# Kernel optimization log

Hardware: AMD Instinct MI355X
Metric: run time of the kernel (lower is better)

The kernel has to match this reference:

```python
import jax, jax.numpy as jnp
import numpy as np

SEGMENT_LENGTHS = [2048, 4096, 8192]
DILATION_RATES = [1, 2, 4]


def setup_inputs() -> dict:
    key = jax.random.key(0)
    kq, kk, kv = jax.random.split(key, 3)
    shape = (4, 8192, 16, 64)  # [b, seq, heads, head_dim]
    return {
        "query": jax.random.normal(kq, shape, dtype=jnp.float32),
        "key": jax.random.normal(kk, shape, dtype=jnp.float32),
        "value": jax.random.normal(kv, shape, dtype=jnp.float32),
    }


def _dilated_attention(query, key, value):
    b, S, h, d = query.shape
    num_groups = len(DILATION_RATES)
    # replicate torch group-size logic: h // ng each, first (h % ng) get +1
    group_sizes = [h // num_groups] * num_groups
    for i in range(h % num_groups):
        group_sizes[i] += 1

    scale = 1.0 / jnp.sqrt(jnp.asarray(d, dtype=query.dtype))
    out = jnp.zeros_like(query)

    for i, (g, r, s) in enumerate(zip(group_sizes, DILATION_RATES, SEGMENT_LENGTHS)):
        n = S // s
        offset = i % r
        hmin, hmax = i * g, (i + 1) * g  # faithful to original (uses current g)

        # gather strided segment views: [b, n, s', g, d]
        q = query.reshape(b, n, s, h, d)[:, :, offset::r, hmin:hmax, :]
        k = key.reshape(b, n, s, h, d)[:, :, offset::r, hmin:hmax, :]
        v = value.reshape(b, n, s, h, d)[:, :, offset::r, hmin:hmax, :]

        # NOTE: the original SDPA is applied to [., s', g, d], so attention
        # runs over the HEAD-group axis (length g) at each position.
        scores = jnp.einsum('bnsqd,bnskd->bnsqk', q, k) * scale
        attn = jax.nn.softmax(scores, axis=-1)
        x = jnp.einsum('bnsqk,bnskd->bnsqd', attn, v)  # [b, n, s', g, d]

        # normalize over (segment, position) dims, as in original
        x = x / x.sum(axis=(1, 2), keepdims=True)

        # scatter-add back into the output buffer
        out5 = out.reshape(b, n, s, h, d)
        out5 = out5.at[:, :, offset::r, hmin:hmax, :].add(x)
        out = out5.reshape(b, S, h, d)

    return out / num_groups


def reference(query, key, value):
    return _dilated_attention(query, key, value)
```

## Files before the change

### kernel.cpp

```cpp
#include <hip/hip_runtime.h>
#include <math.h>

#define BB 4
#define SS 8192
#define HH 16
#define DDIM 64

static const long X0_OFF = 6144;
static const long X0_SZ = 4L * 8192 * 6 * 64;
static const long X1_OFF = X0_OFF + X0_SZ;
static const long X1_SZ = 4L * 4096 * 5 * 64;
static const long X2_OFF = X1_OFF + X1_SZ;
static const long X2_SZ = 4L * 2048 * 5 * 64;
static const long WS_FLOATS = X2_OFF + X2_SZ;

__global__ __launch_bounds__(256) void k_zero_sums(float* ws) {
    int idx = blockIdx.x * 256 + threadIdx.x;
    if (idx < 6144) ws[idx] = 0.0f;
}

__global__ __launch_bounds__(256) void k_recip(float* ws) {
    int idx = blockIdx.x * 256 + threadIdx.x;
    if (idx < 6144) ws[idx] = __frcp_rn(ws[idx]);
}

__device__ __forceinline__ float4 shfl_xor4(float4 v, int m) {
    return make_float4(__shfl_xor(v.x, m, 64), __shfl_xor(v.y, m, 64),
                       __shfl_xor(v.z, m, 64), __shfl_xor(v.w, m, 64));
}

__global__ __launch_bounds__(256) void k_attn(const float* __restrict__ Q,
                                              const float* __restrict__ Kp,
                                              const float* __restrict__ Vp,
                                              float* __restrict__ ws) {
    __shared__ __align__(16) float psum[4][6][64];

    int bid = blockIdx.x;
    int gi, b, tile, g, r, off, hmin, J;
    long xoff;
    if (bid < 2048)      { gi = 0; b = bid >> 9; tile = bid & 511; g = 6; r = 1; off = 0; hmin = 0;  J = 8192; xoff = X0_OFF; }
    else if (bid < 3072) { gi = 1; bid -= 2048; b = bid >> 8; tile = bid & 255; g = 5; r = 2; off = 1; hmin = 5;  J = 4096; xoff = X1_OFF; }
    else                 { gi = 2; bid -= 3072; b = bid >> 7; tile = bid & 127; g = 5; r = 4; off = 2; hmin = 10; J = 2048; xoff = X2_OFF; }

    const int t = threadIdx.x;
    const int lane = t & 63;
    const int wave = t >> 6;
    const int d4 = t & 15;
    const int pIdx = t >> 4;
    const int j = tile * 16 + pIdx;
    const int pos = off + j * r;

    const long rowbase = (((long)b * SS + pos) * HH + hmin) * DDIM;
    const float4* q4p = (const float4*)(Q + rowbase);
    const float4* k4p = (const float4*)(Kp + rowbase);
    const float4* v4p = (const float4*)(Vp + rowbase);

    float4 q4[6], k4[6], v4[6];
#pragma unroll
    for (int hh = 0; hh < 6; ++hh) {
        if (hh < g) {
            q4[hh] = q4p[hh * 16 + d4];
            k4[hh] = k4p[hh * 16 + d4];
            v4[hh] = v4p[hh * 16 + d4];
        } else {
            q4[hh] = make_float4(0.f, 0.f, 0.f, 0.f);
            k4[hh] = q4[hh];
            v4[hh] = q4[hh];
        }
    }

    float p[6][6];
#pragma unroll
    for (int qh = 0; qh < 6; ++qh) {
#pragma unroll
        for (int kh = 0; kh < 6; ++kh) {
            if (qh < g && kh < g) {
                float s = q4[qh].x * k4[kh].x + q4[qh].y * k4[kh].y +
                          q4[qh].z * k4[kh].z + q4[qh].w * k4[kh].w;
#pragma unroll
                for (int m = 1; m <= 8; m <<= 1) s += __shfl_xor(s, m, 64);
                p[qh][kh] = s;
            } else {
                p[qh][kh] = 0.0f;
            }
        }
    }

#pragma unroll
    for (int qh = 0; qh < 6; ++qh) {
        if (qh >= g) continue;
        float mx = -3.4e38f;
#pragma unroll
        for (int kh = 0; kh < 6; ++kh)
            if (kh < g) mx = fmaxf(mx, p[qh][kh]);
        float den = 0.0f;
#pragma unroll
        for (int kh = 0; kh < 6; ++kh) {
            if (kh < g) { p[qh][kh] = __expf((p[qh][kh] - mx) * 0.125f); den += p[qh][kh]; }
        }
        float rden = 1.0f / den;
#pragma unroll
        for (int kh = 0; kh < 6; ++kh) p[qh][kh] *= rden;
    }

    float4* xrow = (float4*)(ws + xoff + (((long)b * J + j) * g) * DDIM);
#pragma unroll
    for (int qh = 0; qh < 6; ++qh) {
        if (qh >= g) continue;
        float4 o = make_float4(0.f, 0.f, 0.f, 0.f);
#pragma unroll
        for (int kh = 0; kh < 6; ++kh) {
            if (kh < g) {
                o.x += p[qh][kh] * v4[kh].x; o.y += p[qh][kh] * v4[kh].y;
                o.z += p[qh][kh] * v4[kh].z; o.w += p[qh][kh] * v4[kh].w;
            }
        }
        xrow[qh * 16 + d4] = o;

        float4 red = o;
        red = shfl_xor4(red, 16);
        {
            float4 tmp = shfl_xor4(red, 32);
            red.x += tmp.x; red.y += tmp.y; red.z += tmp.z; red.w += tmp.w;
        }
        red = o;
#pragma unroll
        for (int m = 16; m <= 32; m <<= 1) {
            float4 tmp = shfl_xor4(red, m);
            red.x += tmp.x; red.y += tmp.y; red.z += tmp.z; red.w += tmp.w;
        }
        if (lane < 16) ((float4*)&psum[wave][qh][0])[d4] = red;
    }
    __syncthreads();

    for (int idx = t; idx < g * 64; idx += 256) {
        int qh = idx >> 6, dd = idx & 63;
        float v = psum[0][qh][dd] + psum[1][qh][dd] + psum[2][qh][dd] + psum[3][qh][dd];
        unsafeAtomicAdd(ws + ((long)(gi * 4 + b) * 8 + qh) * 64 + dd, v);
    }
}

__global__ __launch_bounds__(256) void k_out(const float* __restrict__ ws,
                                             float* __restrict__ out) {
    const int t = threadIdx.x;
    const int bid = blockIdx.x;
    const int dd4 = t & 15;
    const int h = t >> 4;
    const int b = bid >> 10;
    const int pos0 = (bid & 1023) * 8;

    float4 rs0 = make_float4(0.f, 0.f, 0.f, 0.f), rs1 = rs0, rs2 = rs0;
    if (h < 6)
        rs0 = ((const float4*)(ws + ((long)(0 * 4 + b) * 8 + h) * 64))[dd4];
    if (h >= 5 && h <= 9)
        rs1 = ((const float4*)(ws + ((long)(1 * 4 + b) * 8 + (h - 5)) * 64))[dd4];
    if (h >= 10 && h <= 14)
        rs2 = ((const float4*)(ws + ((long)(2 * 4 + b) * 8 + (h - 10)) * 64))[dd4];

#pragma unroll
    for (int pp = 0; pp < 8; ++pp) {
        const int pos = pos0 + pp;
        float4 r = make_float4(0.f, 0.f, 0.f, 0.f);

        if (h < 6) {
            float4 x = ((const float4*)(ws + X0_OFF + (((long)b * 8192 + pos) * 6 + h) * 64))[dd4];
            r.x += x.x * rs0.x; r.y += x.y * rs0.y; r.z += x.z * rs0.z; r.w += x.w * rs0.w;
        }
        if (h >= 5 && h <= 9 && (pos & 1) == 1) {
            int jj = pos >> 1;
            float4 x = ((const float4*)(ws + X1_OFF + (((long)b * 4096 + jj) * 5 + (h - 5)) * 64))[dd4];
            r.x += x.x * rs1.x; r.y += x.y * rs1.y; r.z += x.z * rs1.z; r.w += x.w * rs1.w;
        }
        if (h >= 10 && h <= 14 && (pos & 3) == 2) {
            int jj = pos >> 2;
            float4 x = ((const float4*)(ws + X2_OFF + (((long)b * 2048 + jj) * 5 + (h - 10)) * 64))[dd4];
            r.x += x.x * rs2.x; r.y += x.y * rs2.y; r.z += x.z * rs2.z; r.w += x.w * rs2.w;
        }

        const float third = 1.0f / 3.0f;
        r.x *= third; r.y *= third; r.z *= third; r.w *= third;
        ((float4*)out)[((long)(b * 8192 + pos)) * 256 + t] = r;
    }
}

extern "C" void kernel_launch(void* const* d_in, const int* in_sizes, int n_in,
                              void* d_out, int out_size, void* d_ws, size_t ws_size,
                              hipStream_t stream) {
    const float* Q = (const float*)d_in[0];
    const float* K = (const float*)d_in[1];
    const float* V = (const float*)d_in[2];
    float* ws = (float*)d_ws;
    float* out = (float*)d_out;

    if (ws_size < (size_t)WS_FLOATS * sizeof(float)) return;

    k_zero_sums<<<24, 256, 0, stream>>>(ws);
    k_attn<<<3584, 256, 0, stream>>>(Q, K, V, ws);
    k_recip<<<24, 256, 0, stream>>>(ws);
    k_out<<<4096, 256, 0, stream>>>(ws, out);
}
```

Before: 403.0 us.

## Recompute attention in output kernel instead of materializing intermediates

The first pass now only accumulates the per-(group,batch,head,dim) normalization sums and no longer writes the full attention outputs to workspace. A new fused kernel recomputes the head-group attention per position, applies the reciprocal of the sums (folding the separate reciprocal kernel into it) and writes the final output directly. This trades a large intermediate write plus reread (~40MB each way) for rereading Q/K/V and redoing the small attention arithmetic, and removes one kernel launch.

New measurement: 441.6 us. +9.6%, slower.

```diff
diff --git a/kernel.cpp b/kernel.cpp
--- a/kernel.cpp
+++ b/kernel.cpp
@@ -6,41 +6,29 @@
 #define HH 16
 #define DDIM 64
 
-static const long X0_OFF = 6144;
-static const long X0_SZ = 4L * 8192 * 6 * 64;
-static const long X1_OFF = X0_OFF + X0_SZ;
-static const long X1_SZ = 4L * 4096 * 5 * 64;
-static const long X2_OFF = X1_OFF + X1_SZ;
-static const long X2_SZ = 4L * 2048 * 5 * 64;
-static const long WS_FLOATS = X2_OFF + X2_SZ;
+static const long WS_FLOATS = 6144;
 
 __global__ __launch_bounds__(256) void k_zero_sums(float* ws) {
     int idx = blockIdx.x * 256 + threadIdx.x;
     if (idx < 6144) ws[idx] = 0.0f;
 }
 
-__global__ __launch_bounds__(256) void k_recip(float* ws) {
-    int idx = blockIdx.x * 256 + threadIdx.x;
-    if (idx < 6144) ws[idx] = __frcp_rn(ws[idx]);
-}
-
 __device__ __forceinline__ float4 shfl_xor4(float4 v, int m) {
     return make_float4(__shfl_xor(v.x, m, 64), __shfl_xor(v.y, m, 64),
                        __shfl_xor(v.z, m, 64), __shfl_xor(v.w, m, 64));
 }
 
-__global__ __launch_bounds__(256) void k_attn(const float* __restrict__ Q,
-                                              const float* __restrict__ Kp,
-                                              const float* __restrict__ Vp,
-                                              float* __restrict__ ws) {
+__global__ __launch_bounds__(256) void k_attn_sums(const float* __restrict__ Q,
+                                                   const float* __restrict__ Kp,
+                                                   const float* __restrict__ Vp,
+                                                   float* __restrict__ ws) {
     __shared__ __align__(16) float psum[4][6][64];
 
     int bid = blockIdx.x;
-    int gi, b, tile, g, r, off, hmin, J;
-    long xoff;
-    if (bid < 2048)      { gi = 0; b = bid >> 9; tile = bid & 511; g = 6; r = 1; off = 0; hmin = 0;  J = 8192; xoff = X0_OFF; }
-    else if (bid < 3072) { gi = 1; bid -= 2048; b = bid >> 8; tile = bid & 255; g = 5; r = 2; off = 1; hmin = 5;  J = 4096; xoff = X1_OFF; }
-    else                 { gi = 2; bid -= 3072; b = bid >> 7; tile = bid & 127; g = 5; r = 4; off = 2; hmin = 10; J = 2048; xoff = X2_OFF; }
+    int gi, b, tile, g, r, off, hmin;
+    if (bid < 2048)      { gi = 0; b = bid >> 9; tile = bid & 511; g = 6; r = 1; off = 0; hmin = 0;  }
+    else if (bid < 3072) { gi = 1; bid -= 2048; b = bid >> 8; tile = bid & 255; g = 5; r = 2; off = 1; hmin = 5;  }
+    else                 { gi = 2; bid -= 3072; b = bid >> 7; tile = bid & 127; g = 5; r = 4; off = 2; hmin = 10; }
 
     const int t = threadIdx.x;
     const int lane = t & 63;
@@ -103,7 +91,6 @@
         for (int kh = 0; kh < 6; ++kh) p[qh][kh] *= rden;
     }
 
-    float4* xrow = (float4*)(ws + xoff + (((long)b * J + j) * g) * DDIM);
 #pragma unroll
     for (int qh = 0; qh < 6; ++qh) {
         if (qh >= g) continue;
@@ -115,15 +102,7 @@
                 o.z += p[qh][kh] * v4[kh].z; o.w += p[qh][kh] * v4[kh].w;
             }
         }
-        xrow[qh * 16 + d4] = o;
-
         float4 red = o;
-        red = shfl_xor4(red, 16);
-        {
-            float4 tmp = shfl_xor4(red, 32);
-            red.x += tmp.x; red.y += tmp.y; red.z += tmp.z; red.w += tmp.w;
-        }
-        red = o;
 #pragma unroll
         for (int m = 16; m <= 32; m <<= 1) {
             float4 tmp = shfl_xor4(red, m);
@@ -140,46 +119,123 @@
     }
 }
 
-__global__ __launch_bounds__(256) void k_out(const float* __restrict__ ws,
-                                             float* __restrict__ out) {
+template<int G>
+__device__ __forceinline__ void attn_one(const float* __restrict__ Q,
+                                         const float* __restrict__ Kp,
+                                         const float* __restrict__ Vp,
+                                         long base16, int hmin, int d4,
+                                         float4* o) {
+    const float4* q4p = (const float4*)Q + base16 + (long)hmin * 16;
+    const float4* k4p = (const float4*)Kp + base16 + (long)hmin * 16;
+    const float4* v4p = (const float4*)Vp + base16 + (long)hmin * 16;
+
+    float4 q4[G], k4[G];
+#pragma unroll
+    for (int hh = 0; hh < G; ++hh) {
+        q4[hh] = q4p[hh * 16 + d4];
+        k4[hh] = k4p[hh * 16 + d4];
+    }
+    float p[G][G];
+#pragma unroll
+    for (int qh = 0; qh < G; ++qh)
+#pragma unroll
+        for (int kh = 0; kh < G; ++kh) {
+            float s = q4[qh].x * k4[kh].x + q4[qh].y * k4[kh].y +
+                      q4[qh].z * k4[kh].z + q4[qh].w * k4[kh].w;
+#pragma unroll
+            for (int m = 1; m <= 8; m <<= 1) s += __shfl_xor(s, m, 64);
+            p[qh][kh] = s;
+        }
+#pragma unroll
+    for (int qh = 0; qh < G; ++qh) {
+        float mx = -3.4e38f;
+#pragma unroll
+        for (int kh = 0; kh < G; ++kh) mx = fmaxf(mx, p[qh][kh]);
+        float den = 0.0f;
+#pragma unroll
+        for (int kh = 0; kh < G; ++kh) {
+            p[qh][kh] = __expf((p[qh][kh] - mx) * 0.125f);
+            den += p[qh][kh];
+        }
+        float rden = 1.0f / den;
+#pragma unroll
+        for (int kh = 0; kh < G; ++kh) p[qh][kh] *= rden;
+    }
+    float4 v4[G];
+#pragma unroll
+    for (int kh = 0; kh < G; ++kh) v4[kh] = v4p[kh * 16 + d4];
+#pragma unroll
+    for (int qh = 0; qh < G; ++qh) {
+        float4 acc = make_float4(0.f, 0.f, 0.f, 0.f);
+#pragma unroll
+        for (int kh = 0; kh < G; ++kh) {
+            acc.x += p[qh][kh] * v4[kh].x; acc.y += p[qh][kh] * v4[kh].y;
+            acc.z += p[qh][kh] * v4[kh].z; acc.w += p[qh][kh] * v4[kh].w;
+        }
+        o[qh] = acc;
+    }
+}
+
+__global__ __launch_bounds__(256) void k_fused(const float* __restrict__ Q,
+                                               const float* __restrict__ Kp,
+                                               const float* __restrict__ Vp,
+                                               const float* __restrict__ ws,
+                                               float* __restrict__ out) {
+    __shared__ __align__(16) float rsm[3][6][64];
+
     const int t = threadIdx.x;
     const int bid = blockIdx.x;
-    const int dd4 = t & 15;
-    const int h = t >> 4;
-    const int b = bid >> 10;
-    const int pos0 = (bid & 1023) * 8;
-
-    float4 rs0 = make_float4(0.f, 0.f, 0.f, 0.f), rs1 = rs0, rs2 = rs0;
-    if (h < 6)
-        rs0 = ((const float4*)(ws + ((long)(0 * 4 + b) * 8 + h) * 64))[dd4];
-    if (h >= 5 && h <= 9)
-        rs1 = ((const float4*)(ws + ((long)(1 * 4 + b) * 8 + (h - 5)) * 64))[dd4];
-    if (h >= 10 && h <= 14)
-        rs2 = ((const float4*)(ws + ((long)(2 * 4 + b) * 8 + (h - 10)) * 64))[dd4];
-
-#pragma unroll
-    for (int pp = 0; pp < 8; ++pp) {
-        const int pos = pos0 + pp;
-        float4 r = make_float4(0.f, 0.f, 0.f, 0.f);
-
-        if (h < 6) {
-            float4 x = ((const float4*)(ws + X0_OFF + (((long)b * 8192 + pos) * 6 + h) * 64))[dd4];
-            r.x += x.x * rs0.x; r.y += x.y * rs0.y; r.z += x.z * rs0.z; r.w += x.w * rs0.w;
-        }
-        if (h >= 5 && h <= 9 && (pos & 1) == 1) {
-            int jj = pos >> 1;
-            float4 x = ((const float4*)(ws + X1_OFF + (((long)b * 4096 + jj) * 5 + (h - 5)) * 64))[dd4];
-            r.x += x.x * rs1.x; r.y += x.y * rs1.y; r.z += x.z * rs1.z; r.w += x.w * rs1.w;
-        }
-        if (h >= 10 && h <= 14 && (pos & 3) == 2) {
-            int jj = pos >> 2;
-            float4 x = ((const float4*)(ws + X2_OFF + (((long)b * 2048 + jj) * 5 + (h - 10)) * 64))[dd4];
-            r.x += x.x * rs2.x; r.y += x.y * rs2.y; r.z += x.z * rs2.z; r.w += x.w * rs2.w;
-        }
-
-        const float third = 1.0f / 3.0f;
-        r.x *= third; r.y *= third; r.z *= third; r.w *= third;
-        ((float4*)out)[((long)(b * 8192 + pos)) * 256 + t] = r;
+    const int b = bid >> 9;
+    const int pos0 = (bid & 511) * 16;
+
+    for (int i = t; i < 3 * 6 * 64; i += 256) {
+        const int gi = i / 384, rem = i - gi * 384;
+        const int qh = rem >> 6, dd = rem & 63;
+        rsm[gi][qh][dd] = __frcp_rn(ws[((long)(gi * 4 + b) * 8 + qh) * 64 + dd]);
+    }
+    __syncthreads();
+
+    const int d4 = t & 15;
+    const int pIdx = t >> 4;
+    const int pos = pos0 + pIdx;
+    const bool odd = (pos & 1) == 1;
+    const bool m42 = (pos & 3) == 2;
+    const long base16 = ((long)b * SS + pos) * HH * 16;
+
+    float4 o0[6], o1[5], o2[5];
+#pragma unroll
+    for (int i = 0; i < 5; ++i) { o1[i] = make_float4(0.f, 0.f, 0.f, 0.f); o2[i] = o1[i]; }
+
+    attn_one<6>(Q, Kp, Vp, base16, 0, d4, o0);
+    if (odd) attn_one<5>(Q, Kp, Vp, base16, 5, d4, o1);
+    if (m42) attn_one<5>(Q, Kp, Vp, base16, 10, d4, o2);
+
+    const float third = 1.0f / 3.0f;
+    float4* orow = (float4*)out + base16;
+#pragma unroll
+    for (int h = 0; h < 16; ++h) {
+        float4 rcp, x;
+        bool have = false;
+        if (h < 5) {
+            rcp = ((const float4*)&rsm[0][h][0])[d4]; x = o0[h]; have = true;
+        } else if (h == 5) {
+            rcp = ((const float4*)&rsm[0][5][0])[d4]; x = o0[5]; have = true;
+        } else if (h < 10) {
+            rcp = ((const float4*)&rsm[1][h - 5][0])[d4]; x = o1[h - 5]; have = odd;
+        } else if (h < 15) {
+            rcp = ((const float4*)&rsm[2][h - 10][0])[d4]; x = o2[h - 10]; have = m42;
+        }
+        float4 st = make_float4(0.f, 0.f, 0.f, 0.f);
+        if (have) {
+            st.x = x.x * rcp.x * third; st.y = x.y * rcp.y * third;
+            st.z = x.z * rcp.z * third; st.w = x.w * rcp.w * third;
+        }
+        if (h == 5 && odd) {
+            float4 r1 = ((const float4*)&rsm[1][0][0])[d4];
+            st.x += o1[0].x * r1.x * third; st.y += o1[0].y * r1.y * third;
+            st.z += o1[0].z * r1.z * third; st.w += o1[0].w * r1.w * third;
+        }
+        orow[h * 16 + d4] = st;
     }
 }
 
@@ -195,7 +251,6 @@
     if (ws_size < (size_t)WS_FLOATS * sizeof(float)) return;
 
     k_zero_sums<<<24, 256, 0, stream>>>(ws);
-    k_attn<<<3584, 256, 0, stream>>>(Q, K, V, ws);
-    k_recip<<<24, 256, 0, stream>>>(ws);
-    k_out<<<4096, 256, 0, stream>>>(ws, out);
-}
+    k_attn_sums<<<3584, 256, 0, stream>>>(Q, K, V, ws);
+    k_fused<<<2048, 256, 0, stream>>>(Q, K, V, ws, out);
+}
```
